# Optimization experiments

Measured on AMD Instinct MI355X. Metric: run time of the kernel, lower is better.

## Reference

```python
import jax, jax.numpy as jnp
import numpy as np

N, IN, C, H, NC, E, G = 4096, 16, 128, 2, 4, 131072, 64
EPS = 1e-5


def setup_inputs() -> dict:
    key = jax.random.key(0)
    ks = jax.random.split(key, 12)
    def rn(k, shape, scale=0.05):
        return jax.random.normal(k, shape, dtype=jnp.float32) * scale
    return dict(
        x=rn(ks[0], (N, IN), 1.0),
        edge_index=jax.random.randint(ks[1], (2, E), 0, N, dtype=jnp.int32),
        batch=jnp.sort(jax.random.randint(ks[2], (N,), 0, G, dtype=jnp.int32)),
        proj_W=rn(ks[3], (IN, C)), proj_b=jnp.zeros((C,), jnp.float32),
        gcn_W=rn(ks[4], (2, C, C)), gcn_b=jnp.zeros((2, C), jnp.float32),
        attn_qkv_w=rn(ks[5], (2, 3 * C, C)), attn_qkv_b=jnp.zeros((2, 3 * C), jnp.float32),
        attn_out_w=rn(ks[6], (2, C, C)), attn_out_b=jnp.zeros((2, C), jnp.float32),
        bn_gamma=jnp.ones((2, 3, C), jnp.float32), bn_beta=jnp.zeros((2, 3, C), jnp.float32),
        mlp_W1=rn(ks[7], (2, C, 2 * C)), mlp_b1=jnp.zeros((2, 2 * C), jnp.float32),
        mlp_W2=rn(ks[8], (2, 2 * C, C)), mlp_b2=jnp.zeros((2, C), jnp.float32),
        lin_W=rn(ks[9], (C, NC)), lin_b=jnp.zeros((NC,), jnp.float32),
    )


def _bn(h, g, b):
    # PyG BatchNorm (training-mode stats over the node dim, biased var)
    mu = jnp.mean(h, axis=0)
    var = jnp.mean((h - mu) ** 2, axis=0)
    return (h - mu) * jax.lax.rsqrt(var + EPS) * g + b


def _gcn(h_in, W, b, src, dst):
    # GCNConv: x' = D^-1/2 (A+I) D^-1/2 (x W) + b
    h = h_in @ W
    deg = jnp.zeros((N,), h.dtype).at[dst].add(1.0) + 1.0  # +1 self loop
    dinv = jax.lax.rsqrt(deg)
    coef = dinv[src] * dinv[dst]                           # [E]
    out = jax.ops.segment_sum(h[src] * coef[:, None], dst, num_segments=N)
    out = out + h * (dinv * dinv)[:, None]                 # self-loop term
    return out + b


def _mha(x, wqkv, bqkv, wout, bout):
    # batch=None in the source => attention over all N nodes as one sequence
    qkv = x @ wqkv.T + bqkv                                # [N,3C]
    q, k, v = jnp.split(qkv, 3, axis=-1)
    dh = C // H
    q = q.reshape(N, H, dh) * (dh ** -0.5)
    k = k.reshape(N, H, dh)
    v = v.reshape(N, H, dh)
    a = jax.nn.softmax(jnp.einsum('nhd,mhd->hnm', q, k), axis=-1)  # [H,N,N]
    o = jnp.einsum('hnm,mhd->nhd', a, v).reshape(N, C)
    return o @ wout.T + bout


def _forward(x, proj_W, proj_b, gcn_W, gcn_b, attn_qkv_w, attn_qkv_b,
             attn_out_w, attn_out_b, bn_gamma, bn_beta, mlp_W1, mlp_b1,
             mlp_W2, mlp_b2, lin_W, lin_b, edge_index, batch):
    src, dst = edge_index[0], edge_index[1]
    h = x @ proj_W + proj_b
    for l in range(2):  # two structurally-distinct GPS layers
        hl = _bn(_gcn(h, gcn_W[l], gcn_b[l], src, dst) + h, bn_gamma[l, 0], bn_beta[l, 0])
        ha = _bn(_mha(h, attn_qkv_w[l], attn_qkv_b[l], attn_out_w[l], attn_out_b[l]) + h,
                 bn_gamma[l, 1], bn_beta[l, 1])
        o = hl + ha
        m = jax.nn.relu(o @ mlp_W1[l] + mlp_b1[l]) @ mlp_W2[l] + mlp_b2[l]
        h = _bn(o + m, bn_gamma[l, 2], bn_beta[l, 2])
        if l == 0:
            h = jax.nn.relu(h)
    ssum = jax.ops.segment_sum(h, batch, num_segments=G)
    cnt = jax.ops.segment_sum(jnp.ones((N,), h.dtype), batch, num_segments=G)
    pooled = ssum / jnp.maximum(cnt, 1.0)[:, None]
    return pooled @ lin_W + lin_b


def reference(x, edge_index, batch, proj_W, proj_b, gcn_W, gcn_b,
              attn_qkv_w, attn_qkv_b, attn_out_w, attn_out_b,
              bn_gamma, bn_beta, mlp_W1, mlp_b1, mlp_W2, mlp_b2,
              lin_W, lin_b):
    return _forward(x, proj_W, proj_b, gcn_W, gcn_b, attn_qkv_w, attn_qkv_b,
                    attn_out_w, attn_out_b, bn_gamma, bn_beta, mlp_W1, mlp_b1,
                    mlp_W2, mlp_b2, lin_W, lin_b, edge_index, batch)
```

## Files before the change

kernel.cpp:

```cpp
#include <hip/hip_runtime.h>
#include <hip/hip_bf16.h>


constexpr int N_  = 4096;
constexpr int IN_ = 16;
constexpr int C_  = 128;
constexpr int E_  = 131072;
constexpr int G_  = 64;
constexpr float EPSV = 1e-5f;

typedef unsigned short u16;
typedef __attribute__((ext_vector_type(8))) short bf16x8;
typedef __attribute__((ext_vector_type(8))) unsigned short u16x8;
typedef __attribute__((ext_vector_type(4))) float f32x4;

__device__ inline u16 f2bf(float f) {
  union { __hip_bfloat16 b; u16 u; } v;
  v.b = __float2bfloat16(f);
  return v.u;
}
__device__ inline float bf2f(u16 s) {
  union { unsigned u; float f; } v; v.u = ((unsigned)s) << 16;
  return v.f;
}

__global__ __launch_bounds__(256) void proj_k(const float* __restrict__ x,
                                              const float* __restrict__ W,
                                              const float* __restrict__ b,
                                              float* __restrict__ h) {
  int idx = blockIdx.x * 256 + threadIdx.x;
  int n = idx >> 7, c = idx & 127;
  float acc = b[c];
#pragma unroll
  for (int k = 0; k < IN_; ++k) acc = fmaf(x[n * IN_ + k], W[k * C_ + c], acc);
  h[idx] = acc;
}

__global__ __launch_bounds__(256) void count_k(const int* __restrict__ ei,
                                               int* __restrict__ cnt) {
  int e = blockIdx.x * 256 + threadIdx.x;
  atomicAdd(&cnt[ei[E_ + e]], 1);
}
__global__ __launch_bounds__(256) void scan_k(const int* __restrict__ cnt,
                                              int* __restrict__ rowptr,
                                              int* __restrict__ cursor,
                                              float* __restrict__ dinv) {
  __shared__ int part[256];
  const int t = threadIdx.x;
  int v[16], s = 0;
#pragma unroll
  for (int i = 0; i < 16; ++i) { v[i] = cnt[t * 16 + i]; s += v[i]; }
  part[t] = s;
  __syncthreads();
  if (t == 0) {
    int run = 0;
    for (int i = 0; i < 256; ++i) { int x = part[i]; part[i] = run; run += x; }
  }
  __syncthreads();
  int off = part[t];
#pragma unroll
  for (int i = 0; i < 16; ++i) {
    int n = t * 16 + i;
    rowptr[n] = off; cursor[n] = off;
    dinv[n] = rsqrtf((float)v[i] + 1.0f);
    off += v[i];
  }
  if (t == 0) rowptr[N_] = E_;
}
__global__ __launch_bounds__(256) void fill_k(const int* __restrict__ ei,
                                              int* __restrict__ cursor,
                                              int* __restrict__ csr) {
  int e = blockIdx.x * 256 + threadIdx.x;
  int d = ei[E_ + e];
  int slot = atomicAdd(&cursor[d], 1);
  csr[slot] = ei[e];
}

__global__ __launch_bounds__(256) void wprep_k(const float* __restrict__ gcnW,
                                               const float* __restrict__ qkvW,
                                               const float* __restrict__ outW,
                                               const float* __restrict__ w1,
                                               const float* __restrict__ w2,
                                               u16* __restrict__ Wh,
                                               u16* __restrict__ Wl) {
  int bx = blockIdx.x;
  int l = bx / 144, b = bx % 144;
  const float* src; int dstOff, K, M, trans;
  if (b < 16)       { src = gcnW + l * 16384; dstOff = 0;      K = 128; M = 128; trans = 0; }
  else if (b < 64)  { src = qkvW + l * 49152; dstOff = 16384;  K = 128; M = 0;   trans = 1; b -= 16; }
  else if (b < 80)  { src = outW + l * 16384; dstOff = 65536;  K = 128; M = 0;   trans = 1; b -= 64; }
  else if (b < 112) { src = w1 + l * 32768;   dstOff = 81920;  K = 128; M = 256; trans = 0; b -= 80; }
  else              { src = w2 + l * 32768;   dstOff = 114688; K = 256; M = 128; trans = 0; b -= 112; }
  dstOff += l * 147456;
  int d = b * 1024 + threadIdx.x * 4;
  float v[4];
  if (trans) {
    const float4 f = *(const float4*)&src[d];
    v[0] = f.x; v[1] = f.y; v[2] = f.z; v[3] = f.w;
  } else {
    int ks = (K == 256) ? 8 : 7;
    int n = d >> ks, k = d & (K - 1);
#pragma unroll
    for (int j = 0; j < 4; ++j) v[j] = src[(size_t)(k + j) * M + n];
  }
  ushort4 hv, lv;
  u16* hp = (u16*)&hv; u16* lp = (u16*)&lv;
#pragma unroll
  for (int j = 0; j < 4; ++j) {
    u16 hh = f2bf(v[j]); hp[j] = hh; lp[j] = f2bf(v[j] - bf2f(hh));
  }
  *(ushort4*)&Wh[dstOff + d] = hv;
  *(ushort4*)&Wl[dstOff + d] = lv;
}

__global__ __launch_bounds__(256) void mgemm_dual_k(const float* __restrict__ A,
                                                    const u16* __restrict__ Bh,
                                                    const u16* __restrict__ Bl,
                                                    const float* __restrict__ qkvB,
                                                    float* __restrict__ t0,
                                                    u16* __restrict__ Qg,
                                                    u16* __restrict__ Kg,
                                                    u16* __restrict__ Vtg) {
  constexpr int LD = 72, K = 128;
  __shared__ u16 Ah[64 * LD], Al[64 * LD], Bsh[64 * LD], Bsl[64 * LD];
  const int tid = threadIdx.x;
  const int row0 = blockIdx.y * 64, col0 = blockIdx.x * 64;
  const int wv = tid >> 6, ln = tid & 63, quad = ln >> 4, c = ln & 15;
  f32x4 acc[4];
#pragma unroll
  for (int i = 0; i < 4; ++i) acc[i] = (f32x4){0.f, 0.f, 0.f, 0.f};

  for (int kt = 0; kt < K; kt += 64) {
    __syncthreads();
#pragma unroll
    for (int i = 0; i < 2; ++i) {
      int ch = tid + i * 256, r = ch >> 3, part = ch & 7;
      const float4 f0 = *(const float4*)&A[(size_t)(row0 + r) * K + kt + part * 8];
      const float4 f1 = *(const float4*)&A[(size_t)(row0 + r) * K + kt + part * 8 + 4];
      float fv[8] = {f0.x, f0.y, f0.z, f0.w, f1.x, f1.y, f1.z, f1.w};
      __attribute__((aligned(16))) u16 hb[8], lb[8];
#pragma unroll
      for (int j = 0; j < 8; ++j) {
        u16 hh = f2bf(fv[j]); hb[j] = hh; lb[j] = f2bf(fv[j] - bf2f(hh));
      }
      *(u16x8*)&Ah[r * LD + part * 8] = *(u16x8*)hb;
      *(u16x8*)&Al[r * LD + part * 8] = *(u16x8*)lb;
      size_t bo = (size_t)(col0 + r) * K + kt + part * 8;
      *(u16x8*)&Bsh[r * LD + part * 8] = *(const u16x8*)&Bh[bo];
      *(u16x8*)&Bsl[r * LD + part * 8] = *(const u16x8*)&Bl[bo];
    }
    __syncthreads();
#pragma unroll
    for (int kq = 0; kq < 2; ++kq) {
      bf16x8 ah = *(const bf16x8*)&Ah[(wv * 16 + c) * LD + kq * 32 + quad * 8];
      bf16x8 al = *(const bf16x8*)&Al[(wv * 16 + c) * LD + kq * 32 + quad * 8];
#pragma unroll
      for (int cb = 0; cb < 4; ++cb) {
        bf16x8 bh = *(const bf16x8*)&Bsh[(cb * 16 + c) * LD + kq * 32 + quad * 8];
        bf16x8 bl = *(const bf16x8*)&Bsl[(cb * 16 + c) * LD + kq * 32 + quad * 8];
        acc[cb] = __builtin_amdgcn_mfma_f32_16x16x32_bf16(al, bh, acc[cb], 0, 0, 0);
        acc[cb] = __builtin_amdgcn_mfma_f32_16x16x32_bf16(ah, bl, acc[cb], 0, 0, 0);
        acc[cb] = __builtin_amdgcn_mfma_f32_16x16x32_bf16(ah, bh, acc[cb], 0, 0, 0);
      }
    }
  }

  const int cls = blockIdx.x;
  if (cls < 2) {
#pragma unroll
    for (int cb = 0; cb < 4; ++cb)
#pragma unroll
      for (int r = 0; r < 4; ++r) {
        int rr = row0 + wv * 16 + quad * 4 + r;
        t0[(size_t)rr * 128 + col0 + cb * 16 + c] = acc[cb][r];
      }
  } else if (cls < 6) {
    const int isQ = cls < 4, h = cls & 1;
    const float sc = isQ ? 0.125f : 1.0f;
    u16* dst = isQ ? Qg : Kg;
#pragma unroll
    for (int cb = 0; cb < 4; ++cb) {
      int d = cb * 16 + c;
      float qb = qkvB[col0 - 128 + d];
#pragma unroll
      for (int r = 0; r < 4; ++r) {
        int rr = row0 + wv * 16 + quad * 4 + r;
        dst[((size_t)(h * N_ + rr)) * 64 + d] = f2bf((acc[cb][r] + qb) * sc);
      }
    }
  } else {
    const int h = cls & 1;
    u16* vtile = Ah;
    __syncthreads();
#pragma unroll
    for (int cb = 0; cb < 4; ++cb) {
      int d = cb * 16 + c;
      float vb = qkvB[col0 - 128 + d];
#pragma unroll
      for (int r = 0; r < 4; ++r)
        vtile[(wv * 16 + quad * 4 + r) * LD + d] = f2bf(acc[cb][r] + vb);
    }
    __syncthreads();
    int d = tid >> 2, j = tid & 3;
    __attribute__((aligned(16))) u16 buf[16];
#pragma unroll
    for (int m = 0; m < 16; ++m) buf[m] = vtile[(j * 16 + m) * LD + d];
    size_t o = ((size_t)(h * 64 + d)) * N_ + row0 + j * 16;
    *(u16x8*)&Vtg[o]     = *(u16x8*)&buf[0];
    *(u16x8*)&Vtg[o + 8] = *(u16x8*)&buf[8];
  }
}

__global__ __launch_bounds__(256) void mgemm_k(const float* __restrict__ A,
                                               const u16* __restrict__ Bh,
                                               const u16* __restrict__ Bl,
                                               const float* __restrict__ bias,
                                               float* __restrict__ Cout,
                                               int K, int Ncols, int relu,
                                               const float* __restrict__ resid,
                                               float* __restrict__ sums) {
  constexpr int LD = 72;
  __shared__ u16 Ah[64 * LD], Al[64 * LD], Bsh[64 * LD], Bsl[64 * LD];
  const int tid = threadIdx.x;
  const int row0 = blockIdx.y * 64, col0 = blockIdx.x * 64;
  const int wv = tid >> 6, ln = tid & 63, quad = ln >> 4, c = ln & 15;
  f32x4 acc[4];
#pragma unroll
  for (int i = 0; i < 4; ++i) acc[i] = (f32x4){0.f, 0.f, 0.f, 0.f};

  for (int kt = 0; kt < K; kt += 64) {
    __syncthreads();
#pragma unroll
    for (int i = 0; i < 2; ++i) {
      int ch = tid + i * 256, r = ch >> 3, part = ch & 7;
      const float4 f0 = *(const float4*)&A[(size_t)(row0 + r) * K + kt + part * 8];
      const float4 f1 = *(const float4*)&A[(size_t)(row0 + r) * K + kt + part * 8 + 4];
      float fv[8] = {f0.x, f0.y, f0.z, f0.w, f1.x, f1.y, f1.z, f1.w};
      __attribute__((aligned(16))) u16 hb[8], lb[8];
#pragma unroll
      for (int j = 0; j < 8; ++j) {
        u16 hh = f2bf(fv[j]); hb[j] = hh; lb[j] = f2bf(fv[j] - bf2f(hh));
      }
      *(u16x8*)&Ah[r * LD + part * 8] = *(u16x8*)hb;
      *(u16x8*)&Al[r * LD + part * 8] = *(u16x8*)lb;
      size_t bo = (size_t)(col0 + r) * K + kt + part * 8;
      *(u16x8*)&Bsh[r * LD + part * 8] = *(const u16x8*)&Bh[bo];
      *(u16x8*)&Bsl[r * LD + part * 8] = *(const u16x8*)&Bl[bo];
    }
    __syncthreads();
#pragma unroll
    for (int kq = 0; kq < 2; ++kq) {
      bf16x8 ah = *(const bf16x8*)&Ah[(wv * 16 + c) * LD + kq * 32 + quad * 8];
      bf16x8 al = *(const bf16x8*)&Al[(wv * 16 + c) * LD + kq * 32 + quad * 8];
#pragma unroll
      for (int cb = 0; cb < 4; ++cb) {
        bf16x8 bh = *(const bf16x8*)&Bsh[(cb * 16 + c) * LD + kq * 32 + quad * 8];
        bf16x8 bl = *(const bf16x8*)&Bsl[(cb * 16 + c) * LD + kq * 32 + quad * 8];
        acc[cb] = __builtin_amdgcn_mfma_f32_16x16x32_bf16(al, bh, acc[cb], 0, 0, 0);
        acc[cb] = __builtin_amdgcn_mfma_f32_16x16x32_bf16(ah, bl, acc[cb], 0, 0, 0);
        acc[cb] = __builtin_amdgcn_mfma_f32_16x16x32_bf16(ah, bh, acc[cb], 0, 0, 0);
      }
    }
  }
#pragma unroll
  for (int cb = 0; cb < 4; ++cb) {
    float s = 0.0f, s2 = 0.0f;
#pragma unroll
    for (int r = 0; r < 4; ++r) {
      int rr = row0 + wv * 16 + quad * 4 + r;
      int cc = col0 + cb * 16 + c;
      float o = acc[cb][r] + (bias ? bias[cc] : 0.0f);
      if (resid) o += resid[(size_t)rr * Ncols + cc];
      if (relu) o = fmaxf(o, 0.0f);
      Cout[(size_t)rr * Ncols + cc] = o;
      s += o; s2 = fmaf(o, o, s2);
    }
    if (sums) {
      s  += __shfl_xor(s, 16);  s  += __shfl_xor(s, 32);
      s2 += __shfl_xor(s2, 16); s2 += __shfl_xor(s2, 32);
      if (quad == 0) {
        int cc = col0 + cb * 16 + c;
        atomicAdd(&sums[cc], s);
        atomicAdd(&sums[C_ + cc], s2);
      }
    }
  }
}

__global__ __launch_bounds__(256) void mgemm_attn_k(const float* __restrict__ attnP,
                                                    const float* __restrict__ accLp,
                                                    const u16* __restrict__ Bh,
                                                    const u16* __restrict__ Bl,
                                                    const float* __restrict__ bias,
                                                    float* __restrict__ Cout,
                                                    const float* __restrict__ resid,
                                                    float* __restrict__ sums) {
  constexpr int LD = 72, K = 128;
  __shared__ u16 Ah[64 * LD], Al[64 * LD], Bsh[64 * LD], Bsl[64 * LD];
  const int tid = threadIdx.x;
  const int row0 = blockIdx.y * 64, col0 = blockIdx.x * 64;
  const int wv = tid >> 6, ln = tid & 63, quad = ln >> 4, c = ln & 15;
  f32x4 acc[4];
#pragma unroll
  for (int i = 0; i < 4; ++i) acc[i] = (f32x4){0.f, 0.f, 0.f, 0.f};

  for (int kt = 0; kt < K; kt += 64) {
    const int head = kt >> 6;
    __syncthreads();
#pragma unroll
    for (int i = 0; i < 2; ++i) {
      int ch = tid + i * 256, r = ch >> 3, part = ch & 7;
      float lsum = 0.0f;
#pragma unroll
      for (int sp = 0; sp < 8; ++sp) lsum += accLp[(sp * 2 + head) * N_ + row0 + r];
      float invl = 1.0f / lsum;
      float fv[8] = {0.f, 0.f, 0.f, 0.f, 0.f, 0.f, 0.f, 0.f};
#pragma unroll
      for (int sp = 0; sp < 8; ++sp) {
        const float* p = &attnP[((size_t)sp * N_ + row0 + r) * C_ + kt + part * 8];
        const float4 f0 = *(const float4*)p;
        const float4 f1 = *(const float4*)(p + 4);
        fv[0] += f0.x; fv[1] += f0.y; fv[2] += f0.z; fv[3] += f0.w;
        fv[4] += f1.x; fv[5] += f1.y; fv[6] += f1.z; fv[7] += f1.w;
      }
      __attribute__((aligned(16))) u16 hb[8], lb[8];
#pragma unroll
      for (int j = 0; j < 8; ++j) {
        float f = fv[j] * invl;
        u16 hh = f2bf(f); hb[j] = hh; lb[j] = f2bf(f - bf2f(hh));
      }
      *(u16x8*)&Ah[r * LD + part * 8] = *(u16x8*)hb;
      *(u16x8*)&Al[r * LD + part * 8] = *(u16x8*)lb;
      size_t bo = (size_t)(col0 + r) * K + kt + part * 8;
      *(u16x8*)&Bsh[r * LD + part * 8] = *(const u16x8*)&Bh[bo];
      *(u16x8*)&Bsl[r * LD + part * 8] = *(const u16x8*)&Bl[bo];
    }
    __syncthreads();
#pragma unroll
    for (int kq = 0; kq < 2; ++kq) {
      bf16x8 ah = *(const bf16x8*)&Ah[(wv * 16 + c) * LD + kq * 32 + quad * 8];
      bf16x8 al = *(const bf16x8*)&Al[(wv * 16 + c) * LD + kq * 32 + quad * 8];
#pragma unroll
      for (int cb = 0; cb < 4; ++cb) {
        bf16x8 bh = *(const bf16x8*)&Bsh[(cb * 16 + c) * LD + kq * 32 + quad * 8];
        bf16x8 bl = *(const bf16x8*)&Bsl[(cb * 16 + c) * LD + kq * 32 + quad * 8];
        acc[cb] = __builtin_amdgcn_mfma_f32_16x16x32_bf16(al, bh, acc[cb], 0, 0, 0);
        acc[cb] = __builtin_amdgcn_mfma_f32_16x16x32_bf16(ah, bl, acc[cb], 0, 0, 0);
        acc[cb] = __builtin_amdgcn_mfma_f32_16x16x32_bf16(ah, bh, acc[cb], 0, 0, 0);
      }
    }
  }
#pragma unroll
  for (int cb = 0; cb < 4; ++cb) {
    float s = 0.0f, s2 = 0.0f;
#pragma unroll
    for (int r = 0; r < 4; ++r) {
      int rr = row0 + wv * 16 + quad * 4 + r;
      int cc = col0 + cb * 16 + c;
      float o = acc[cb][r] + bias[cc] + resid[(size_t)rr * 128 + cc];
      Cout[(size_t)rr * 128 + cc] = o;
      s += o; s2 = fmaf(o, o, s2);
    }
    s  += __shfl_xor(s, 16);  s  += __shfl_xor(s, 32);
    s2 += __shfl_xor(s2, 16); s2 += __shfl_xor(s2, 32);
    if (quad == 0) {
      int cc = col0 + cb * 16 + c;
      atomicAdd(&sums[cc], s);
      atomicAdd(&sums[C_ + cc], s2);
    }
  }
}

__global__ __launch_bounds__(128) void gcn_gather_k(const int* __restrict__ rowptr,
                                                    const int* __restrict__ csr,
                                                    const float* __restrict__ hw,
                                                    const float* __restrict__ dinv,
                                                    const float* __restrict__ b,
                                                    const float* __restrict__ hres,
                                                    float* __restrict__ out) {
  const int n = blockIdx.x, c = threadIdx.x;
  const float din = dinv[n];
  float acc = fmaf(hw[(size_t)n * C_ + c], din * din, b[c] + hres[(size_t)n * C_ + c]);
  const int e1 = rowptr[n + 1];
  for (int e = rowptr[n]; e < e1; ++e) {
    int s = csr[e];
    acc = fmaf(hw[(size_t)s * C_ + c], dinv[s] * din, acc);
  }
  out[(size_t)n * C_ + c] = acc;
}

__global__ __launch_bounds__(256) void bn_stats_k(const float* __restrict__ A,
                                                  float* __restrict__ sums) {
  int c = threadIdx.x & 127, half = threadIdx.x >> 7;
  int r0 = blockIdx.x * 16 + half * 8;
  float s = 0.0f, s2 = 0.0f;
#pragma unroll
  for (int i = 0; i < 8; ++i) {
    float v = A[(size_t)(r0 + i) * C_ + c];
    s += v;
    s2 = fmaf(v, v, s2);
  }
  __shared__ float ls[256], ls2[256];
  ls[threadIdx.x] = s; ls2[threadIdx.x] = s2;
  __syncthreads();
  if (half == 0) {
    atomicAdd(&sums[c], s + ls[c + 128]);
    atomicAdd(&sums[C_ + c], s2 + ls2[c + 128]);
  }
}

__global__ __launch_bounds__(256) void bn_finapply2_k(const float* __restrict__ t0,
                                                      const float* __restrict__ t1,
                                                      const float* __restrict__ sums1,
                                                      const float* __restrict__ sums0,
                                                      const float* __restrict__ g1,
                                                      const float* __restrict__ b1v,
                                                      const float* __restrict__ g0,
                                                      const float* __restrict__ b0v,
                                                      float* __restrict__ ob) {
  __shared__ float scl1[128], shf1[128], scl0[128], shf0[128];
  const int t = threadIdx.x;
  if (t < 128) {
    float mu = sums1[t] * (1.0f / N_);
    float var = sums1[C_ + t] * (1.0f / N_) - mu * mu;
    float sc = rsqrtf(var + EPSV) * g1[t];
    scl1[t] = sc; shf1[t] = fmaf(-mu, sc, b1v[t]);
    mu = sums0[t] * (1.0f / N_);
    var = sums0[C_ + t] * (1.0f / N_) - mu * mu;
    sc = rsqrtf(var + EPSV) * g0[t];
    scl0[t] = sc; shf0[t] = fmaf(-mu, sc, b0v[t]);
  }
  __syncthreads();
  int idx = blockIdx.x * 256 + t;
  int c = idx & 127;
  ob[idx] = fmaf(t0[idx], scl1[c], shf1[c]) + fmaf(t1[idx], scl0[c], shf0[c]);
}

__global__ __launch_bounds__(256) void bn_finapply_k(const float* __restrict__ A,
                                                     const float* __restrict__ sums,
                                                     const float* __restrict__ g,
                                                     const float* __restrict__ b,
                                                     float* __restrict__ outp, int relu,
                                                     const int* __restrict__ batch,
                                                     float* __restrict__ pooled) {
  __shared__ float s_scl[128], s_shf[128];
  const int t = threadIdx.x;
  if (t < 128) {
    float mu = sums[t] * (1.0f / N_);
    float var = sums[C_ + t] * (1.0f / N_) - mu * mu;
    float sc = rsqrtf(var + EPSV) * g[t];
    s_scl[t] = sc;
    s_shf[t] = fmaf(-mu, sc, b[t]);
  }
  __syncthreads();
  int idx = blockIdx.x * 256 + t;
  int c = idx & 127;
  float v = fmaf(A[idx], s_scl[c], s_shf[c]);
  if (relu) v = fmaxf(v, 0.0f);
  outp[idx] = v;
  if (pooled) {
    int n = idx >> 7;
    atomicAdd(&pooled[(size_t)batch[n] * C_ + c], v);
  }
}

__global__ __launch_bounds__(256) void flash_mfma_k(const u16* __restrict__ Qg,
                                                    const u16* __restrict__ Kg,
                                                    const u16* __restrict__ Vtg,
                                                    float* __restrict__ attnP,
                                                    float* __restrict__ accLp) {
  constexpr int LD = 72;
  __shared__ u16 Ks[64 * LD], Vts[64 * LD], Ps[64 * LD];
  const int tid = threadIdx.x;
  const int h = blockIdx.z, sp = blockIdx.y, q0 = blockIdx.x * 64;
  const int wv = tid >> 6, ln = tid & 63, quad = ln >> 4, c = ln & 15;

  bf16x8 qf[2];
#pragma unroll
  for (int kq = 0; kq < 2; ++kq)
    qf[kq] = *(const bf16x8*)&Qg[((size_t)(h * N_ + q0 + wv * 16 + c)) * 64 + kq * 32 + quad * 8];

  f32x4 O[4];
#pragma unroll
  for (int i = 0; i < 4; ++i) O[i] = (f32x4){0.f, 0.f, 0.f, 0.f};
  float l4[4] = {0.f, 0.f, 0.f, 0.f};
  u16* Pw = &Ps[wv * 16 * LD];

  for (int it = 0; it < 8; ++it) {
    const int k0 = sp * 512 + it * 64;
    __syncthreads();
#pragma unroll
    for (int i = 0; i < 2; ++i) {
      int ch = tid + i * 256, row = ch >> 3, part = ch & 7;
      *(u16x8*)&Ks[row * LD + part * 8] =
          *(const u16x8*)&Kg[((size_t)(h * N_ + k0 + row)) * 64 + part * 8];
      *(u16x8*)&Vts[row * LD + part * 8] =
          *(const u16x8*)&Vtg[((size_t)(h * 64 + row)) * N_ + k0 + part * 8];
    }
    __syncthreads();

#pragma unroll
    for (int kb = 0; kb < 4; ++kb) {
      f32x4 s = (f32x4){0.f, 0.f, 0.f, 0.f};
#pragma unroll
      for (int kq = 0; kq < 2; ++kq) {
        bf16x8 b = *(const bf16x8*)&Ks[(kb * 16 + c) * LD + kq * 32 + quad * 8];
        s = __builtin_amdgcn_mfma_f32_16x16x32_bf16(qf[kq], b, s, 0, 0, 0);
      }
#pragma unroll
      for (int r = 0; r < 4; ++r) {
        u16 ph = f2bf(__expf(s[r] - 8.0f));
        l4[r] += bf2f(ph);
        Pw[(quad * 4 + r) * LD + kb * 16 + c] = ph;
      }
    }
#pragma unroll
    for (int db = 0; db < 4; ++db) {
#pragma unroll
      for (int kq = 0; kq < 2; ++kq) {
        bf16x8 a = *(const bf16x8*)&Pw[c * LD + kq * 32 + quad * 8];
        bf16x8 b = *(const bf16x8*)&Vts[(db * 16 + c) * LD + kq * 32 + quad * 8];
        O[db] = __builtin_amdgcn_mfma_f32_16x16x32_bf16(a, b, O[db], 0, 0, 0);
      }
    }
  }

#pragma unroll
  for (int r = 0; r < 4; ++r) {
#pragma unroll
    for (int off = 1; off < 16; off <<= 1) l4[r] += __shfl_xor(l4[r], off);
  }

#pragma unroll
  for (int db = 0; db < 4; ++db)
#pragma unroll
    for (int r = 0; r < 4; ++r) {
      int q = q0 + wv * 16 + quad * 4 + r;
      attnP[((size_t)sp * N_ + q) * C_ + h * 64 + db * 16 + c] = O[db][r];
    }
  if (c == 0) {
#pragma unroll
    for (int r = 0; r < 4; ++r)
      accLp[(sp * 2 + h) * N_ + q0 + wv * 16 + quad * 4 + r] = l4[r];
  }
}

__global__ __launch_bounds__(256) void final_k(const float* __restrict__ pooled,
                                               const int* __restrict__ batch,
                                               const float* __restrict__ W,
                                               const float* __restrict__ b,
                                               float* __restrict__ out) {
  int t = threadIdx.x;
  int g = t >> 2, j = t & 3;
  int lo = 0, hi = N_;
  while (lo < hi) { int m = (lo + hi) >> 1; if (batch[m] < g) lo = m + 1; else hi = m; }
  int st = lo; lo = 0; hi = N_;
  while (lo < hi) { int m = (lo + hi) >> 1; if (batch[m] < g + 1) lo = m + 1; else hi = m; }
  float inv = 1.0f / fmaxf((float)(lo - st), 1.0f);
  float acc = b[j];
  for (int c = 0; c < C_; ++c) acc = fmaf(pooled[(size_t)g * C_ + c] * inv, W[c * 4 + j], acc);
  out[t] = acc;
}

extern "C" void kernel_launch(void* const* d_in, const int* in_sizes, int n_in,
                              void* d_out, int out_size, void* d_ws, size_t ws_size,
                              hipStream_t stream) {
  const float* x     = (const float*)d_in[0];
  const int*   ei    = (const int*)d_in[1];
  const int*   batch = (const int*)d_in[2];
  const float* projW = (const float*)d_in[3];
  const float* projB = (const float*)d_in[4];
  const float* gcnW  = (const float*)d_in[5];
  const float* gcnB  = (const float*)d_in[6];
  const float* qkvW  = (const float*)d_in[7];
  const float* qkvB  = (const float*)d_in[8];
  const float* outW  = (const float*)d_in[9];
  const float* outB  = (const float*)d_in[10];
  const float* bnG   = (const float*)d_in[11];
  const float* bnB   = (const float*)d_in[12];
  const float* w1    = (const float*)d_in[13];
  const float* b1    = (const float*)d_in[14];
  const float* w2    = (const float*)d_in[15];
  const float* b2    = (const float*)d_in[16];
  const float* linW  = (const float*)d_in[17];
  const float* linB  = (const float*)d_in[18];
  float* out = (float*)d_out;

  const size_t NC = (size_t)N_ * C_;
  const size_t HB = (size_t)2 * N_ * 64;
  float* ws   = (float*)d_ws;
  float* h    = ws;
  float* t0   = ws + 1 * NC;
  float* t1   = ws + 2 * NC;
  float* ob   = ws + 3 * NC;
  u16* Qg  = (u16*)(ws + 4 * NC);
  u16* Kg  = Qg + HB;
  u16* Vtg = Kg + HB;
  float* attnP = ws + 6 * NC;
  float* m1b   = attnP;
  float* accLp = ws + 14 * NC;
  float* sums  = accLp + 16 * N_;
  float* pooled = sums + 6 * 256;
  int*   icnt = (int*)(pooled + (size_t)G_ * C_);
  float* dinv = (float*)(icnt + N_);
  int*   rowptr = (int*)(dinv + N_);
  int*   cursor = rowptr + N_ + 1;
  int*   csr    = cursor + N_;
  u16*   Wh = (u16*)(csr + E_);
  u16*   Wl = Wh + 2 * 147456;

  const dim3 b256(256);

  hipMemsetAsync(sums, 0, (6 * 256 + (size_t)G_ * C_ + N_) * sizeof(float), stream);

  count_k<<<E_ / 256, b256, 0, stream>>>(ei, icnt);
  scan_k<<<1, b256, 0, stream>>>(icnt, rowptr, cursor, dinv);
  fill_k<<<E_ / 256, b256, 0, stream>>>(ei, cursor, csr);

  proj_k<<<(int)(NC / 256), b256, 0, stream>>>(x, projW, projB, h);
  wprep_k<<<288, b256, 0, stream>>>(gcnW, qkvW, outW, w1, w2, Wh, Wl);

  for (int l = 0; l < 2; ++l) {
    const size_t WL = (size_t)l * 147456;
    float* sums0 = sums + (l * 3 + 0) * 256;
    float* sums1 = sums + (l * 3 + 1) * 256;
    float* sums2 = sums + (l * 3 + 2) * 256;

    mgemm_dual_k<<<dim3(8, 64), b256, 0, stream>>>(h, Wh + WL, Wl + WL,
                                                   qkvB + l * 384, t0, Qg, Kg, Vtg);
    gcn_gather_k<<<N_, dim3(128), 0, stream>>>(rowptr, csr, t0, dinv, gcnB + l * C_, h, t1);
    bn_stats_k<<<N_ / 16, b256, 0, stream>>>(t1, sums0);
    flash_mfma_k<<<dim3(N_ / 64, 8, 2), b256, 0, stream>>>(Qg, Kg, Vtg, attnP, accLp);
    mgemm_attn_k<<<dim3(2, 64), b256, 0, stream>>>(attnP, accLp,
                                                   Wh + WL + 65536, Wl + WL + 65536,
                                                   outB + l * C_, t0, h, sums1);
    bn_finapply2_k<<<(int)(NC / 256), b256, 0, stream>>>(
        t0, t1, sums1, sums0,
        bnG + (l * 3 + 1) * C_, bnB + (l * 3 + 1) * C_,
        bnG + (l * 3 + 0) * C_, bnB + (l * 3 + 0) * C_, ob);
    mgemm_k<<<dim3(4, 64), b256, 0, stream>>>(ob, Wh + WL + 81920, Wl + WL + 81920,
                                              b1 + l * 256, m1b, 128, 256, 1,
                                              nullptr, nullptr);
    mgemm_k<<<dim3(2, 64), b256, 0, stream>>>(m1b, Wh + WL + 114688, Wl + WL + 114688,
                                              b2 + l * C_, t0, 256, 128, 0,
                                              ob, sums2);
    bn_finapply_k<<<(int)(NC / 256), b256, 0, stream>>>(
        t0, sums2, bnG + (l * 3 + 2) * C_, bnB + (l * 3 + 2) * C_, h,
        (l == 0) ? 1 : 0, batch, (l == 1) ? pooled : nullptr);
  }

  final_k<<<1, 256, 0, stream>>>(pooled, batch, linW, linB, out);
}
```

Measured before the change: 336.5 us.

## Double query rows per flash block and split keys into 16 partitions

Each attention block now handles 128 queries, two 16-row groups per wave, so every K/V tile loaded into shared memory serves twice as many queries. The key dimension is split into 16 partitions instead of 8, which keeps the grid at 1024 blocks. The cost is twice as many partial output and row-sum buffers in the workspace, and the downstream combine in mgemm_attn_k must now read and sum 16 partials instead of 8. Register pressure per wave also rises.

```diff
diff --git a/kernel.cpp b/kernel.cpp
--- a/kernel.cpp
+++ b/kernel.cpp
@@ -8,6 +8,7 @@
 constexpr int E_  = 131072;
 constexpr int G_  = 64;
 constexpr float EPSV = 1e-5f;
+constexpr int SP_ = 16;
 
 typedef unsigned short u16;
 typedef __attribute__((ext_vector_type(8))) short bf16x8;
@@ -312,11 +313,11 @@
       int ch = tid + i * 256, r = ch >> 3, part = ch & 7;
       float lsum = 0.0f;
 #pragma unroll
-      for (int sp = 0; sp < 8; ++sp) lsum += accLp[(sp * 2 + head) * N_ + row0 + r];
+      for (int sp = 0; sp < SP_; ++sp) lsum += accLp[(sp * 2 + head) * N_ + row0 + r];
       float invl = 1.0f / lsum;
       float fv[8] = {0.f, 0.f, 0.f, 0.f, 0.f, 0.f, 0.f, 0.f};
 #pragma unroll
-      for (int sp = 0; sp < 8; ++sp) {
+      for (int sp = 0; sp < SP_; ++sp) {
         const float* p = &attnP[((size_t)sp * N_ + row0 + r) * C_ + kt + part * 8];
         const float4 f0 = *(const float4*)p;
         const float4 f1 = *(const float4*)(p + 4);
@@ -470,24 +471,30 @@
                                                     float* __restrict__ attnP,
                                                     float* __restrict__ accLp) {
   constexpr int LD = 72;
-  __shared__ u16 Ks[64 * LD], Vts[64 * LD], Ps[64 * LD];
+  __shared__ u16 Ks[64 * LD], Vts[64 * LD], Ps[128 * LD];
   const int tid = threadIdx.x;
-  const int h = blockIdx.z, sp = blockIdx.y, q0 = blockIdx.x * 64;
+  const int h = blockIdx.z, sp = blockIdx.y, q0 = blockIdx.x * 128;
   const int wv = tid >> 6, ln = tid & 63, quad = ln >> 4, c = ln & 15;
-
-  bf16x8 qf[2];
-#pragma unroll
-  for (int kq = 0; kq < 2; ++kq)
-    qf[kq] = *(const bf16x8*)&Qg[((size_t)(h * N_ + q0 + wv * 16 + c)) * 64 + kq * 32 + quad * 8];
-
-  f32x4 O[4];
-#pragma unroll
-  for (int i = 0; i < 4; ++i) O[i] = (f32x4){0.f, 0.f, 0.f, 0.f};
-  float l4[4] = {0.f, 0.f, 0.f, 0.f};
-  u16* Pw = &Ps[wv * 16 * LD];
-
-  for (int it = 0; it < 8; ++it) {
-    const int k0 = sp * 512 + it * 64;
+  const int KPS = N_ / SP_;
+
+  bf16x8 qf[2][2];
+#pragma unroll
+  for (int g = 0; g < 2; ++g)
+#pragma unroll
+    for (int kq = 0; kq < 2; ++kq)
+      qf[g][kq] = *(const bf16x8*)
+          &Qg[((size_t)(h * N_ + q0 + wv * 32 + g * 16 + c)) * 64 + kq * 32 + quad * 8];
+
+  f32x4 O[2][4];
+#pragma unroll
+  for (int g = 0; g < 2; ++g)
+#pragma unroll
+    for (int i = 0; i < 4; ++i) O[g][i] = (f32x4){0.f, 0.f, 0.f, 0.f};
+  float l4[2][4] = {};
+  u16* Pw = &Ps[wv * 32 * LD];
+
+  for (int it = 0; it < KPS / 64; ++it) {
+    const int k0 = sp * KPS + it * 64;
     __syncthreads();
 #pragma unroll
     for (int i = 0; i < 2; ++i) {
@@ -500,48 +507,57 @@
     __syncthreads();
 
 #pragma unroll
-    for (int kb = 0; kb < 4; ++kb) {
-      f32x4 s = (f32x4){0.f, 0.f, 0.f, 0.f};
-#pragma unroll
-      for (int kq = 0; kq < 2; ++kq) {
-        bf16x8 b = *(const bf16x8*)&Ks[(kb * 16 + c) * LD + kq * 32 + quad * 8];
-        s = __builtin_amdgcn_mfma_f32_16x16x32_bf16(qf[kq], b, s, 0, 0, 0);
-      }
+    for (int g = 0; g < 2; ++g)
+#pragma unroll
+      for (int kb = 0; kb < 4; ++kb) {
+        f32x4 s = (f32x4){0.f, 0.f, 0.f, 0.f};
+#pragma unroll
+        for (int kq = 0; kq < 2; ++kq) {
+          bf16x8 b = *(const bf16x8*)&Ks[(kb * 16 + c) * LD + kq * 32 + quad * 8];
+          s = __builtin_amdgcn_mfma_f32_16x16x32_bf16(qf[g][kq], b, s, 0, 0, 0);
+        }
+#pragma unroll
+        for (int r = 0; r < 4; ++r) {
+          u16 ph = f2bf(__expf(s[r] - 8.0f));
+          l4[g][r] += bf2f(ph);
+          Pw[(g * 16 + quad * 4 + r) * LD + kb * 16 + c] = ph;
+        }
+      }
+#pragma unroll
+    for (int g = 0; g < 2; ++g)
+#pragma unroll
+      for (int db = 0; db < 4; ++db) {
+#pragma unroll
+        for (int kq = 0; kq < 2; ++kq) {
+          bf16x8 a = *(const bf16x8*)&Pw[(g * 16 + c) * LD + kq * 32 + quad * 8];
+          bf16x8 b = *(const bf16x8*)&Vts[(db * 16 + c) * LD + kq * 32 + quad * 8];
+          O[g][db] = __builtin_amdgcn_mfma_f32_16x16x32_bf16(a, b, O[g][db], 0, 0, 0);
+        }
+      }
+  }
+
+#pragma unroll
+  for (int g = 0; g < 2; ++g)
+#pragma unroll
+    for (int r = 0; r < 4; ++r) {
+#pragma unroll
+      for (int off = 1; off < 16; off <<= 1) l4[g][r] += __shfl_xor(l4[g][r], off);
+    }
+
+#pragma unroll
+  for (int g = 0; g < 2; ++g) {
+#pragma unroll
+    for (int db = 0; db < 4; ++db)
 #pragma unroll
       for (int r = 0; r < 4; ++r) {
-        u16 ph = f2bf(__expf(s[r] - 8.0f));
-        l4[r] += bf2f(ph);
-        Pw[(quad * 4 + r) * LD + kb * 16 + c] = ph;
-      }
-    }
-#pragma unroll
-    for (int db = 0; db < 4; ++db) {
-#pragma unroll
-      for (int kq = 0; kq < 2; ++kq) {
-        bf16x8 a = *(const bf16x8*)&Pw[c * LD + kq * 32 + quad * 8];
-        bf16x8 b = *(const bf16x8*)&Vts[(db * 16 + c) * LD + kq * 32 + quad * 8];
-        O[db] = __builtin_amdgcn_mfma_f32_16x16x32_bf16(a, b, O[db], 0, 0, 0);
-      }
-    }
-  }
-
-#pragma unroll
-  for (int r = 0; r < 4; ++r) {
-#pragma unroll
-    for (int off = 1; off < 16; off <<= 1) l4[r] += __shfl_xor(l4[r], off);
-  }
-
-#pragma unroll
-  for (int db = 0; db < 4; ++db)
-#pragma unroll
-    for (int r = 0; r < 4; ++r) {
-      int q = q0 + wv * 16 + quad * 4 + r;
-      attnP[((size_t)sp * N_ + q) * C_ + h * 64 + db * 16 + c] = O[db][r];
-    }
-  if (c == 0) {
-#pragma unroll
-    for (int r = 0; r < 4; ++r)
-      accLp[(sp * 2 + h) * N_ + q0 + wv * 16 + quad * 4 + r] = l4[r];
+        int q = q0 + wv * 32 + g * 16 + quad * 4 + r;
+        attnP[((size_t)sp * N_ + q) * C_ + h * 64 + db * 16 + c] = O[g][db][r];
+      }
+    if (c == 0) {
+#pragma unroll
+      for (int r = 0; r < 4; ++r)
+        accLp[(sp * 2 + h) * N_ + q0 + wv * 32 + g * 16 + quad * 4 + r] = l4[g][r];
+    }
   }
 }
 
@@ -598,8 +614,8 @@
   u16* Vtg = Kg + HB;
   float* attnP = ws + 6 * NC;
   float* m1b   = attnP;
-  float* accLp = ws + 14 * NC;
-  float* sums  = accLp + 16 * N_;
+  float* accLp = ws + (6 + SP_) * NC;
+  float* sums  = accLp + 2 * SP_ * N_;
   float* pooled = sums + 6 * 256;
   int*   icnt = (int*)(pooled + (size_t)G_ * C_);
   float* dinv = (float*)(icnt + N_);
@@ -630,7 +646,7 @@
                                                    qkvB + l * 384, t0, Qg, Kg, Vtg);
     gcn_gather_k<<<N_, dim3(128), 0, stream>>>(rowptr, csr, t0, dinv, gcnB + l * C_, h, t1);
     bn_stats_k<<<N_ / 16, b256, 0, stream>>>(t1, sums0);
-    flash_mfma_k<<<dim3(N_ / 64, 8, 2), b256, 0, stream>>>(Qg, Kg, Vtg, attnP, accLp);
+    flash_mfma_k<<<dim3(N_ / 128, SP_, 2), b256, 0, stream>>>(Qg, Kg, Vtg, attnP, accLp);
     mgemm_attn_k<<<dim3(2, 64), b256, 0, stream>>>(attnP, accLp,
                                                    Wh + WL + 65536, Wl + WL + 65536,
                                                    outB + l * C_, t0, h, sums1);
```

After: 347.7 us. +3.3%, slower.
